# Kernel optimization log

Measured on AMD Instinct MI355X. Metric: run time of the kernel, lower is better.

## Reference

```python
import jax, jax.numpy as jnp
import numpy as np

T, B, H, OUT = 64, 4096, 256, 2
SLOPE = 25.0  # snntorch surrogate.fast_sigmoid default slope


@jax.custom_vjp
def spike(x):
    # Heaviside forward, fast-sigmoid surrogate gradient backward
    return (x > 0).astype(x.dtype)

def _spk_fwd(x):
    return (x > 0).astype(x.dtype), x

def _spk_bwd(x, g):
    return (g / (SLOPE * jnp.abs(x) + 1.0) ** 2,)

spike.defvjp(_spk_fwd, _spk_bwd)


def temporal_embedding(length):
    center = length // 2
    sigma = length / 10
    pos = np.arange(length)
    e = np.exp(-0.5 * ((pos - center) / sigma) ** 2)
    e = (e - e.min()) / (e.max() - e.min())
    return jnp.asarray(e, dtype=jnp.float32)


def setup_inputs() -> dict:
    key = jax.random.key(0)
    ks = jax.random.split(key, 16)

    def lin(k, o, i):
        bound = 1.0 / np.sqrt(i)
        kw, kb = jax.random.split(k)
        W = jax.random.uniform(kw, (o, i), minval=-bound, maxval=bound, dtype=jnp.float32)
        b = jax.random.uniform(kb, (o,), minval=-bound, maxval=bound, dtype=jnp.float32)
        return W, b

    W_in, b_in = lin(ks[0], H, 3)
    W_h, b_h = lin(ks[1], H, H)
    W_h2, b_h2 = lin(ks[2], H, H)
    W_out, b_out = lin(ks[3], OUT, H)
    W_pred, b_pred = lin(ks[4], OUT, T * 4)
    u = lambda k, n: jax.random.uniform(k, (n,), dtype=jnp.float32)
    return {
        "x": jax.random.normal(ks[5], (T, B, 3), dtype=jnp.float32),
        "W_in": W_in, "b_in": b_in,
        "beta_in": u(ks[6], H), "thr_in": u(ks[7], H),
        "W_h": W_h, "b_h": b_h,
        "beta_h": u(ks[8], H), "thr_h": u(ks[9], H),
        "W_h2": W_h2, "b_h2": b_h2,
        "beta_h2": u(ks[10], H), "thr_h2": u(ks[11], H),
        "W_out": W_out, "b_out": b_out,
        "beta_out": u(ks[12], OUT),
        "W_pred": W_pred, "b_pred": b_pred,
    }


def reference(x, W_in, b_in, beta_in, thr_in, W_h, b_h, beta_h, thr_h,
              W_h2, b_h2, beta_h2, thr_h2, W_out, b_out, beta_out,
              W_pred, b_pred):
    Tn, Bsz = x.shape[0], x.shape[1]
    emb = temporal_embedding(Tn)
    x = x * emb[:, None, None]  # per-timestep Gaussian temporal weighting

    def lif(cur, mem, beta, thr):
        # snnTorch Leaky, reset_mechanism='subtract': reset from PREVIOUS mem (detached)
        reset = jax.lax.stop_gradient((mem - thr > 0).astype(cur.dtype))
        mem = jnp.clip(beta, 0.0, 1.0) * mem + cur - reset * thr
        return spike(mem - thr), mem

    def step(carry, x_t):
        m1, m2, m4, m3 = carry
        s1, m1 = lif(x_t @ W_in.T + b_in, m1, beta_in, thr_in)
        s2, m2 = lif(s1 @ W_h.T + b_h, m2, beta_h, thr_h)
        s4, m4 = lif(s2 @ W_h2.T + b_h2, m4, beta_h2, thr_h2)
        # li_out: reset_mechanism='none', default threshold=1.0
        m3 = jnp.clip(beta_out, 0.0, 1.0) * m3 + s4 @ W_out.T + b_out
        spk_out = spike(m3 - 1.0)
        return (m1, m2, m4, m3), (spk_out, m3)

    z = lambda n: jnp.zeros((Bsz, n), x.dtype)
    init = (z(W_in.shape[0]), z(W_h.shape[0]), z(W_h2.shape[0]), z(W_out.shape[0]))
    _, (spk_rec, mem_rec) = jax.lax.scan(step, init, x)
    out = jnp.concatenate([spk_rec, mem_rec], axis=-1)  # [T, B, 2*OUT]
    # torch .view(B, T*2*OUT) on contiguous [T,B,2*OUT] == plain reshape
    out = out.reshape(Bsz, Tn * out.shape[-1])
    return out @ W_pred.T + b_pred  # [B, OUT]
```

## Files before the change

### kernel.cpp

```cpp
#include <hip/hip_runtime.h>
#include <hip/hip_bf16.h>

#define TT 64
#define BB 4096
#define HH 256
#define BMb 16
#define NBLK (BB / BMb)

typedef short bf16x8_t __attribute__((ext_vector_type(8)));
typedef float f32x4_t  __attribute__((ext_vector_type(4)));

#define WS_WA_B   0u
#define WS_EMB_B  786432u
#define WS_REC_B  1048576u

__device__ __forceinline__ float clip01f(float v) {
    return fminf(fmaxf(v, 0.0f), 1.0f);
}

__global__ __launch_bounds__(64) void setup_emb_kernel(float* __restrict__ emb) {
    int i = threadIdx.x;
    const double sigma = 64.0 / 10.0;
    const double c = 32.0;
    double d = ((double)i - c) / sigma;
    double e = exp(-0.5 * (d * d));
    double d0 = (0.0 - c) / sigma;
    double emin = exp(-0.5 * (d0 * d0));
    emb[i] = (float)((e - emin) / (1.0 - emin));
}

__global__ __launch_bounds__(256) void split_weights_kernel(
    const float* __restrict__ W_h, const float* __restrict__ W_h2,
    unsigned short* __restrict__ WA)
{
    int flat = blockIdx.x * 256 + threadIdx.x;
    int j     = flat & 7;
    int lane  = (flat >> 3) & 63;
    int ntile = (flat >> 9) & 15;
    int kt    = (flat >> 13) & 7;
    int rest  = flat >> 16;
    int part  = rest % 3;
    int layer = rest / 3;
    int k = kt * 32 + (lane >> 4) * 8 + j;
    int n = ntile * 16 + (lane & 15);
    const float* W = layer ? W_h2 : W_h;
    float w = W[n * HH + k];
    __hip_bfloat16 h = __float2bfloat16(w);
    float r1 = w - __bfloat162float(h);
    __hip_bfloat16 m = __float2bfloat16(r1);
    float r2 = r1 - __bfloat162float(m);
    __hip_bfloat16 l = __float2bfloat16(r2);
    __hip_bfloat16 v = (part == 0) ? h : ((part == 1) ? m : l);
    WA[flat] = *reinterpret_cast<unsigned short*>(&v);
}

union U16x8 { uint4 u; bf16x8_t v; };


#define AS1 __attribute__((address_space(1)))
#define AS3 __attribute__((address_space(3)))
__device__ __forceinline__ void gl16(const void* g, void* l) {
    __builtin_amdgcn_global_load_lds((AS1 const void*)g, (AS3 void*)l, 16, 0, 0);
}

#define ISSUE6(Wc, ktn, sl) do {                                               \
    const char* gb_ = (const char*)(Wc) + (ktn) * 16384;                       \
    char* lb_ = myring + (sl) * 6144;                                          \
    gl16(gb_,          lb_);                                                   \
    gl16(gb_ + 1024,   lb_ + 1024);                                            \
    gl16(gb_ + 131072, lb_ + 2048);                                            \
    gl16(gb_ + 132096, lb_ + 3072);                                            \
    gl16(gb_ + 262144, lb_ + 4096);                                            \
    gl16(gb_ + 263168, lb_ + 5120);                                            \
} while (0)

#define STEPD2(sl, Bp, ktb, Wi, kti, D0, D1) do {                              \
    asm volatile("s_waitcnt vmcnt(6)" ::: "memory");                           \
    __builtin_amdgcn_sched_barrier(0);                                         \
    U16x8 br_, a0_, a1_, a2_, b0_, b1_, b2_;                                   \
    br_.u = (Bp)[(ktb) * 64];                               \
    a0_.u = ringRd[(sl) * 384 + 0];                                            \
    b0_.u = ringRd[(sl) * 384 + 64];                                           \
    a1_.u = ringRd[(sl) * 384 + 128];                                          \
    b1_.u = ringRd[(sl) * 384 + 192];                                          \
    a2_.u = ringRd[(sl) * 384 + 256];                                          \
    b2_.u = ringRd[(sl) * 384 + 320];                                          \
    asm volatile("s_waitcnt lgkmcnt(0)" ::: "memory");                         \
    __builtin_amdgcn_sched_barrier(0);                                         \
    ISSUE6(Wi, kti, sl);                                                       \
    __builtin_amdgcn_sched_barrier(0);                                         \
    D0 = __builtin_amdgcn_mfma_f32_16x16x32_bf16(a0_.v, br_.v, D0, 0, 0, 0);   \
    D0 = __builtin_amdgcn_mfma_f32_16x16x32_bf16(a1_.v, br_.v, D0, 0, 0, 0);   \
    D0 = __builtin_amdgcn_mfma_f32_16x16x32_bf16(a2_.v, br_.v, D0, 0, 0, 0);   \
    D1 = __builtin_amdgcn_mfma_f32_16x16x32_bf16(b0_.v, br_.v, D1, 0, 0, 0);   \
    D1 = __builtin_amdgcn_mfma_f32_16x16x32_bf16(b1_.v, br_.v, D1, 0, 0, 0);   \
    D1 = __builtin_amdgcn_mfma_f32_16x16x32_bf16(b2_.v, br_.v, D1, 0, 0, 0);   \
} while (0)

#define GPHASE(Wc, Wn, Bp, D0, D1) do {                                        \
    STEPD2(0, Bp, 0, Wc, 2, D0, D1);                                           \
    STEPD2(1, Bp, 1, Wc, 3, D0, D1);                                           \
    STEPD2(0, Bp, 2, Wc, 4, D0, D1);                                           \
    STEPD2(1, Bp, 3, Wc, 5, D0, D1);                                           \
    STEPD2(0, Bp, 4, Wc, 6, D0, D1);                                           \
    STEPD2(1, Bp, 5, Wc, 7, D0, D1);                                           \
    STEPD2(0, Bp, 6, Wn, 0, D0, D1);                                           \
    STEPD2(1, Bp, 7, Wn, 1, D0, D1);                                           \
} while (0)

__device__ __forceinline__ void li_walker(
    const float* __restrict__ WoutS, const float (*__restrict__ S3F)[260],
    int wb, int ooc, float bto, float bo, float& m3s,
    float* __restrict__ rec, int t, int b0, int lane)
{
    if (lane < 32) {
        const float* wrow = WoutS + ooc * HH;
        const float* srow = S3F[wb];
        float p = 0.f;
#pragma unroll 8
        for (int k4 = 0; k4 < 64; ++k4) {
            float4 sv = *(const float4*)(srow + k4 * 4);
            float4 wv = *(const float4*)(wrow + k4 * 4);
            p = fmaf(sv.x, wv.x, p);
            p = fmaf(sv.y, wv.y, p);
            p = fmaf(sv.z, wv.z, p);
            p = fmaf(sv.w, wv.w, p);
        }
        float mm3 = fmaf(bto, m3s, p);
        mm3 = mm3 + bo;
        m3s = mm3;
        float spk = ((m3s - 1.0f) > 0.f) ? 1.f : 0.f;
        float om3 = __shfl_xor(m3s, 16, 64);
        float osp = __shfl_xor(spk, 16, 64);
        if (lane < 16) {
            *(float4*)(rec + ((size_t)t * BB + b0 + wb) * 4) =
                make_float4(spk, osp, m3s, om3);
        }
    }
}

__global__ __launch_bounds__(512) void snn_main_kernel(
    const float* __restrict__ x,
    const float* __restrict__ W_in, const float* __restrict__ b_in,
    const float* __restrict__ beta_in, const float* __restrict__ thr_in,
    const float* __restrict__ b_h, const float* __restrict__ beta_h, const float* __restrict__ thr_h,
    const float* __restrict__ b_h2, const float* __restrict__ beta_h2, const float* __restrict__ thr_h2,
    const float* __restrict__ W_out, const float* __restrict__ b_out, const float* __restrict__ beta_out,
    const unsigned short* __restrict__ WA, const float* __restrict__ emb,
    float* __restrict__ rec)
{
#pragma clang fp contract(off)
    const int tid = threadIdx.x;
    const int w = tid >> 6;
    const int lane = tid & 63;
    const int b = lane & 15;
    const int g = lane >> 4;
    const int b0 = blockIdx.x * BMb;

    __shared__ unsigned short sbuf1[8 * 64 * 8];
    __shared__ unsigned short sbuf2[8 * 64 * 8];
    __shared__ __align__(16) float S3F[16][260];
    __shared__ __align__(16) float WoutS[2 * HH];
    __shared__ float4 PL1a[HH];
    __shared__ float2 PL1b[HH];
    __shared__ float4 PL2[HH];
    __shared__ float4 PL3[HH];
    __shared__ float  xs[TT][BMb][3];
    __shared__ float  embS[TT];
    __shared__ __align__(16) char ring[8 * 2 * 6144];

    char* myring = ring + w * 12288;
    const uint4* ringRd = (const uint4*)(ring + w * 12288 + lane * 16);

    WoutS[tid] = W_out[tid];
    if (tid < HH) {
        int n = tid;
        PL1a[n] = make_float4(W_in[n * 3], W_in[n * 3 + 1], W_in[n * 3 + 2], b_in[n]);
        PL1b[n] = make_float2(clip01f(beta_in[n]), thr_in[n]);
        PL2[n]  = make_float4(b_h[n],  clip01f(beta_h[n]),  thr_h[n],  0.f);
        PL3[n]  = make_float4(b_h2[n], clip01f(beta_h2[n]), thr_h2[n], 0.f);
    }
    if (tid < TT) embS[tid] = emb[tid];
#pragma unroll
    for (int i = tid; i < TT * BMb; i += 512) {
        int ts = i >> 4, bb = i & 15;
        const float* xp = x + ((size_t)ts * BB + b0 + bb) * 3;
        xs[ts][bb][0] = xp[0];
        xs[ts][bb][1] = xp[1];
        xs[ts][bb][2] = xp[2];
    }

    const int nb0 = w * 32 + g * 4;

    float m1[2][4], m2[2][4], m4[2][4];
#pragma unroll
    for (int u = 0; u < 2; ++u)
#pragma unroll
        for (int r = 0; r < 4; ++r) { m1[u][r] = 0.f; m2[u][r] = 0.f; m4[u][r] = 0.f; }

    const int sb0 = ((w * 64 + ((g >> 1) * 16 + b)) * 8 + (g & 1) * 4);

    const int wb = lane & 15;
    const int ooc = (lane >> 4) & 1;
    float bto = clip01f(beta_out[ooc]);
    float bo = b_out[ooc];
    float m3s = 0.f;

    const uint4* W2 = (const uint4*)WA + (size_t)(2 * w) * 64 + lane;
    const uint4* W3 = W2 + 24576;
    const uint4* Bp1 = (const uint4*)sbuf1 + lane;
    const uint4* Bp2 = (const uint4*)sbuf2 + lane;

    ISSUE6(W2, 0, 0);
    ISSUE6(W2, 1, 1);

    __syncthreads();

    for (int t = 0; t < TT; ++t) {
        {
            float et = embS[t];
            float xe0 = xs[t][b][0] * et;
            float xe1 = xs[t][b][1] * et;
            float xe2 = xs[t][b][2] * et;
            unsigned sp[2][4];
#pragma unroll
            for (int u = 0; u < 2; ++u)
#pragma unroll
            for (int r = 0; r < 4; ++r) {
                int n = nb0 + u * 16 + r;
                float4 pa = PL1a[n];
                float2 pb = PL1b[n];
                float a1 = xe0 * pa.x;
                a1 = fmaf(xe1, pa.y, a1);
                a1 = fmaf(xe2, pa.z, a1);
                float cur = a1 + pa.w;
                float rf = ((m1[u][r] - pb.y) > 0.f) ? 1.f : 0.f;
                float mm = fmaf(pb.x, m1[u][r], cur);
                mm = fmaf(-rf, pb.y, mm);
                m1[u][r] = mm;
                sp[u][r] = ((mm - pb.y) > 0.f) ? 0x3F80u : 0u;
            }
            *(uint2*)(sbuf1 + sb0)       = make_uint2(sp[0][0] | (sp[0][1] << 16), sp[0][2] | (sp[0][3] << 16));
            *(uint2*)(sbuf1 + sb0 + 256) = make_uint2(sp[1][0] | (sp[1][1] << 16), sp[1][2] | (sp[1][3] << 16));
        }
        __syncthreads();

        if (w == 0 && t > 0)
            li_walker(WoutS, S3F, wb, ooc, bto, bo, m3s, rec, t - 1, b0, lane);
        {
            f32x4_t D0 = (f32x4_t){0.f, 0.f, 0.f, 0.f};
            f32x4_t D1 = (f32x4_t){0.f, 0.f, 0.f, 0.f};
            GPHASE(W2, W3, Bp1, D0, D1);
            unsigned sp[2][4];
#pragma unroll
            for (int r = 0; r < 4; ++r) {
                int n0 = nb0 + r;
                float4 p2 = PL2[n0];
                float cur = D0[r] + p2.x;
                float rf = ((m2[0][r] - p2.z) > 0.f) ? 1.f : 0.f;
                float mm = fmaf(p2.y, m2[0][r], cur);
                mm = fmaf(-rf, p2.z, mm);
                m2[0][r] = mm;
                sp[0][r] = ((mm - p2.z) > 0.f) ? 0x3F80u : 0u;
            }
#pragma unroll
            for (int r = 0; r < 4; ++r) {
                int n1 = nb0 + 16 + r;
                float4 p2 = PL2[n1];
                float cur = D1[r] + p2.x;
                float rf = ((m2[1][r] - p2.z) > 0.f) ? 1.f : 0.f;
                float mm = fmaf(p2.y, m2[1][r], cur);
                mm = fmaf(-rf, p2.z, mm);
                m2[1][r] = mm;
                sp[1][r] = ((mm - p2.z) > 0.f) ? 0x3F80u : 0u;
            }
            *(uint2*)(sbuf2 + sb0)       = make_uint2(sp[0][0] | (sp[0][1] << 16), sp[0][2] | (sp[0][3] << 16));
            *(uint2*)(sbuf2 + sb0 + 256) = make_uint2(sp[1][0] | (sp[1][1] << 16), sp[1][2] | (sp[1][3] << 16));
        }
        __syncthreads();

        {
            f32x4_t E0 = (f32x4_t){0.f, 0.f, 0.f, 0.f};
            f32x4_t E1 = (f32x4_t){0.f, 0.f, 0.f, 0.f};
            GPHASE(W3, W2, Bp2, E0, E1);
            float s3v[2][4];
#pragma unroll
            for (int r = 0; r < 4; ++r) {
                int n0 = nb0 + r;
                float4 p3 = PL3[n0];
                float cur = E0[r] + p3.x;
                float rf = ((m4[0][r] - p3.z) > 0.f) ? 1.f : 0.f;
                float mm = fmaf(p3.y, m4[0][r], cur);
                mm = fmaf(-rf, p3.z, mm);
                m4[0][r] = mm;
                s3v[0][r] = ((mm - p3.z) > 0.f) ? 1.0f : 0.0f;
            }
#pragma unroll
            for (int r = 0; r < 4; ++r) {
                int n1 = nb0 + 16 + r;
                float4 p3 = PL3[n1];
                float cur = E1[r] + p3.x;
                float rf = ((m4[1][r] - p3.z) > 0.f) ? 1.f : 0.f;
                float mm = fmaf(p3.y, m4[1][r], cur);
                mm = fmaf(-rf, p3.z, mm);
                m4[1][r] = mm;
                s3v[1][r] = ((mm - p3.z) > 0.f) ? 1.0f : 0.0f;
            }
            *(float4*)(&S3F[b][nb0])      = make_float4(s3v[0][0], s3v[0][1], s3v[0][2], s3v[0][3]);
            *(float4*)(&S3F[b][nb0 + 16]) = make_float4(s3v[1][0], s3v[1][1], s3v[1][2], s3v[1][3]);
        }
        __syncthreads();
    }

    if (w == 0)
        li_walker(WoutS, S3F, wb, ooc, bto, bo, m3s, rec, TT - 1, b0, lane);
}

__global__ __launch_bounds__(256) void pred_kernel(
    const float* __restrict__ rec, const float* __restrict__ W_pred,
    const float* __restrict__ b_pred, float* __restrict__ out)
{
#pragma clang fp contract(off)
    int r = blockIdx.x * 256 + threadIdx.x;
    const float* f = rec + (size_t)r * 256;
    float a0 = 0.f, a1 = 0.f;
#pragma unroll 4
    for (int c = 0; c < 256; ++c) {
        float v = f[c];
        a0 = fmaf(v, W_pred[c], a0);
        a1 = fmaf(v, W_pred[256 + c], a1);
    }
    out[r * 2 + 0] = a0 + b_pred[0];
    out[r * 2 + 1] = a1 + b_pred[1];
}

extern "C" void kernel_launch(void* const* d_in, const int* in_sizes, int n_in,
                              void* d_out, int out_size, void* d_ws, size_t ws_size,
                              hipStream_t stream)
{
    const float* x        = (const float*)d_in[0];
    const float* W_in     = (const float*)d_in[1];
    const float* b_in     = (const float*)d_in[2];
    const float* beta_in  = (const float*)d_in[3];
    const float* thr_in   = (const float*)d_in[4];
    const float* W_h      = (const float*)d_in[5];
    const float* b_h      = (const float*)d_in[6];
    const float* beta_h   = (const float*)d_in[7];
    const float* thr_h    = (const float*)d_in[8];
    const float* W_h2     = (const float*)d_in[9];
    const float* b_h2     = (const float*)d_in[10];
    const float* beta_h2  = (const float*)d_in[11];
    const float* thr_h2   = (const float*)d_in[12];
    const float* W_out    = (const float*)d_in[13];
    const float* b_out    = (const float*)d_in[14];
    const float* beta_out = (const float*)d_in[15];
    const float* W_pred   = (const float*)d_in[16];
    const float* b_pred   = (const float*)d_in[17];

    char* ws = (char*)d_ws;
    unsigned short* WA = (unsigned short*)(ws + WS_WA_B);
    float* emb = (float*)(ws + WS_EMB_B);
    float* rec = (float*)(ws + WS_REC_B);

    split_weights_kernel<<<1536, 256, 0, stream>>>(W_h, W_h2, WA);
    setup_emb_kernel<<<1, 64, 0, stream>>>(emb);

    snn_main_kernel<<<NBLK, 512, 0, stream>>>(
        x, W_in, b_in, beta_in, thr_in,
        b_h, beta_h, thr_h,
        b_h2, beta_h2, thr_h2,
        W_out, b_out, beta_out,
        WA, emb, rec);

    pred_kernel<<<BB / 256, 256, 0, stream>>>(rec, W_pred, b_pred, (float*)d_out);
}
```

Before: 741.9 us.

## Batch four timesteps per weight stream and pack layer-3 spikes as ballot bitmasks

Processes timesteps in chunks of four so that each weight tile streamed from global memory into the LDS ring is reused for four MFMA sets. This amortises weight traffic and cuts the number of barriers per step. Layer-3 spikes are now stored as wave ballot bitmasks rather than a float matrix, and the output LI walker decodes those bits serially, four timesteps at a time. The costs are more accumulator registers, an extra barrier per chunk, and a slower scalar bit-decoding loop in wave 0.

```diff
diff --git a/kernel.cpp b/kernel.cpp
--- a/kernel.cpp
+++ b/kernel.cpp
@@ -6,6 +6,8 @@
 #define HH 256
 #define BMb 16
 #define NBLK (BB / BMb)
+#define TC 4
+#define NCH (TT / TC)
 
 typedef short bf16x8_t __attribute__((ext_vector_type(8)));
 typedef float f32x4_t  __attribute__((ext_vector_type(4)));
@@ -74,57 +76,58 @@
     gl16(gb_ + 263168, lb_ + 5120);                                            \
 } while (0)
 
-#define STEPD2(sl, Bp, ktb, Wi, kti, D0, D1) do {                              \
+#define STEPT(sl, ktb, Wi, kti) do {                                           \
     asm volatile("s_waitcnt vmcnt(6)" ::: "memory");                           \
     __builtin_amdgcn_sched_barrier(0);                                         \
-    U16x8 br_, a0_, a1_, a2_, b0_, b1_, b2_;                                   \
-    br_.u = (Bp)[(ktb) * 64];                               \
-    a0_.u = ringRd[(sl) * 384 + 0];                                            \
-    b0_.u = ringRd[(sl) * 384 + 64];                                           \
-    a1_.u = ringRd[(sl) * 384 + 128];                                          \
-    b1_.u = ringRd[(sl) * 384 + 192];                                          \
-    a2_.u = ringRd[(sl) * 384 + 256];                                          \
-    b2_.u = ringRd[(sl) * 384 + 320];                                          \
+    U16x8 wa0_, wa1_, wa2_, wb0_, wb1_, wb2_;                                  \
+    wa0_.u = ringRd[(sl) * 384 + 0];                                           \
+    wb0_.u = ringRd[(sl) * 384 + 64];                                          \
+    wa1_.u = ringRd[(sl) * 384 + 128];                                         \
+    wb1_.u = ringRd[(sl) * 384 + 192];                                         \
+    wa2_.u = ringRd[(sl) * 384 + 256];                                         \
+    wb2_.u = ringRd[(sl) * 384 + 320];                                         \
     asm volatile("s_waitcnt lgkmcnt(0)" ::: "memory");                         \
     __builtin_amdgcn_sched_barrier(0);                                         \
     ISSUE6(Wi, kti, sl);                                                       \
     __builtin_amdgcn_sched_barrier(0);                                         \
-    D0 = __builtin_amdgcn_mfma_f32_16x16x32_bf16(a0_.v, br_.v, D0, 0, 0, 0);   \
-    D0 = __builtin_amdgcn_mfma_f32_16x16x32_bf16(a1_.v, br_.v, D0, 0, 0, 0);   \
-    D0 = __builtin_amdgcn_mfma_f32_16x16x32_bf16(a2_.v, br_.v, D0, 0, 0, 0);   \
-    D1 = __builtin_amdgcn_mfma_f32_16x16x32_bf16(b0_.v, br_.v, D1, 0, 0, 0);   \
-    D1 = __builtin_amdgcn_mfma_f32_16x16x32_bf16(b1_.v, br_.v, D1, 0, 0, 0);   \
-    D1 = __builtin_amdgcn_mfma_f32_16x16x32_bf16(b2_.v, br_.v, D1, 0, 0, 0);   \
+    _Pragma("unroll")                                                          \
+    for (int tt_ = 0; tt_ < TC; ++tt_) {                                       \
+        U16x8 br_; br_.u = BfL[tt_ * 512 + (ktb) * 64];                        \
+        D0[tt_] = __builtin_amdgcn_mfma_f32_16x16x32_bf16(wa0_.v, br_.v, D0[tt_], 0, 0, 0); \
+        D0[tt_] = __builtin_amdgcn_mfma_f32_16x16x32_bf16(wa1_.v, br_.v, D0[tt_], 0, 0, 0); \
+        D0[tt_] = __builtin_amdgcn_mfma_f32_16x16x32_bf16(wa2_.v, br_.v, D0[tt_], 0, 0, 0); \
+        D1[tt_] = __builtin_amdgcn_mfma_f32_16x16x32_bf16(wb0_.v, br_.v, D1[tt_], 0, 0, 0); \
+        D1[tt_] = __builtin_amdgcn_mfma_f32_16x16x32_bf16(wb1_.v, br_.v, D1[tt_], 0, 0, 0); \
+        D1[tt_] = __builtin_amdgcn_mfma_f32_16x16x32_bf16(wb2_.v, br_.v, D1[tt_], 0, 0, 0); \
+    }                                                                          \
 } while (0)
 
-#define GPHASE(Wc, Wn, Bp, D0, D1) do {                                        \
-    STEPD2(0, Bp, 0, Wc, 2, D0, D1);                                           \
-    STEPD2(1, Bp, 1, Wc, 3, D0, D1);                                           \
-    STEPD2(0, Bp, 2, Wc, 4, D0, D1);                                           \
-    STEPD2(1, Bp, 3, Wc, 5, D0, D1);                                           \
-    STEPD2(0, Bp, 4, Wc, 6, D0, D1);                                           \
-    STEPD2(1, Bp, 5, Wc, 7, D0, D1);                                           \
-    STEPD2(0, Bp, 6, Wn, 0, D0, D1);                                           \
-    STEPD2(1, Bp, 7, Wn, 1, D0, D1);                                           \
+#define GPHASE(Wc, Wn) do {                                                    \
+    STEPT(0, 0, Wc, 2);                                                        \
+    STEPT(1, 1, Wc, 3);                                                        \
+    STEPT(0, 2, Wc, 4);                                                        \
+    STEPT(1, 3, Wc, 5);                                                        \
+    STEPT(0, 4, Wc, 6);                                                        \
+    STEPT(1, 5, Wc, 7);                                                        \
+    STEPT(0, 6, Wn, 0);                                                        \
+    STEPT(1, 7, Wn, 1);                                                        \
 } while (0)
 
-__device__ __forceinline__ void li_walker(
-    const float* __restrict__ WoutS, const float (*__restrict__ S3F)[260],
+__device__ __forceinline__ void li_walker_bits(
+    const float* __restrict__ WoutS, const unsigned long long (*__restrict__ M3Lt)[4],
     int wb, int ooc, float bto, float bo, float& m3s,
     float* __restrict__ rec, int t, int b0, int lane)
 {
     if (lane < 32) {
-        const float* wrow = WoutS + ooc * HH;
-        const float* srow = S3F[wb];
         float p = 0.f;
-#pragma unroll 8
-        for (int k4 = 0; k4 < 64; ++k4) {
-            float4 sv = *(const float4*)(srow + k4 * 4);
-            float4 wv = *(const float4*)(wrow + k4 * 4);
-            p = fmaf(sv.x, wv.x, p);
-            p = fmaf(sv.y, wv.y, p);
-            p = fmaf(sv.z, wv.z, p);
-            p = fmaf(sv.w, wv.w, p);
+        for (int k = 0; k < HH; ++k) {
+            int ww = k >> 4, gg = (k >> 2) & 3, reg = k & 3;
+            unsigned long long word = M3Lt[ww][reg];
+            unsigned w32 = (gg < 2) ? (unsigned)word : (unsigned)(word >> 32);
+            int sh = ((gg & 1) << 4) | wb;
+            unsigned bit = (w32 >> sh) & 1u;
+            float wv = WoutS[ooc * HH + k];
+            p = p + (bit ? wv : 0.f);
         }
         float mm3 = fmaf(bto, m3s, p);
         mm3 = mm3 + bo;
@@ -157,9 +160,8 @@
     const int g = lane >> 4;
     const int b0 = blockIdx.x * BMb;
 
-    __shared__ unsigned short sbuf1[8 * 64 * 8];
-    __shared__ unsigned short sbuf2[8 * 64 * 8];
-    __shared__ __align__(16) float S3F[16][260];
+    __shared__ __align__(16) unsigned short frag[TC][8 * 64 * 8];
+    __shared__ unsigned long long M3L[TC][16][4];
     __shared__ __align__(16) float WoutS[2 * HH];
     __shared__ float4 PL1a[HH];
     __shared__ float2 PL1b[HH];
@@ -171,6 +173,7 @@
 
     char* myring = ring + w * 12288;
     const uint4* ringRd = (const uint4*)(ring + w * 12288 + lane * 16);
+    const uint4* BfL = (const uint4*)frag + lane;
 
     WoutS[tid] = W_out[tid];
     if (tid < HH) {
@@ -208,16 +211,19 @@
 
     const uint4* W2 = (const uint4*)WA + (size_t)(2 * w) * 64 + lane;
     const uint4* W3 = W2 + 24576;
-    const uint4* Bp1 = (const uint4*)sbuf1 + lane;
-    const uint4* Bp2 = (const uint4*)sbuf2 + lane;
 
     ISSUE6(W2, 0, 0);
     ISSUE6(W2, 1, 1);
 
     __syncthreads();
 
-    for (int t = 0; t < TT; ++t) {
-        {
+#pragma unroll 1
+    for (int c = 0; c < NCH; ++c) {
+        const int t0 = c * TC;
+
+#pragma unroll
+        for (int tt = 0; tt < TC; ++tt) {
+            const int t = t0 + tt;
             float et = embS[t];
             float xe0 = xs[t][b][0] * et;
             float xe1 = xs[t][b][1] * et;
@@ -240,23 +246,35 @@
                 m1[u][r] = mm;
                 sp[u][r] = ((mm - pb.y) > 0.f) ? 0x3F80u : 0u;
             }
-            *(uint2*)(sbuf1 + sb0)       = make_uint2(sp[0][0] | (sp[0][1] << 16), sp[0][2] | (sp[0][3] << 16));
-            *(uint2*)(sbuf1 + sb0 + 256) = make_uint2(sp[1][0] | (sp[1][1] << 16), sp[1][2] | (sp[1][3] << 16));
+            *(uint2*)(&frag[tt][sb0])       = make_uint2(sp[0][0] | (sp[0][1] << 16), sp[0][2] | (sp[0][3] << 16));
+            *(uint2*)(&frag[tt][sb0 + 256]) = make_uint2(sp[1][0] | (sp[1][1] << 16), sp[1][2] | (sp[1][3] << 16));
         }
         __syncthreads();
 
-        if (w == 0 && t > 0)
-            li_walker(WoutS, S3F, wb, ooc, bto, bo, m3s, rec, t - 1, b0, lane);
-        {
-            f32x4_t D0 = (f32x4_t){0.f, 0.f, 0.f, 0.f};
-            f32x4_t D1 = (f32x4_t){0.f, 0.f, 0.f, 0.f};
-            GPHASE(W2, W3, Bp1, D0, D1);
+        if (w == 0 && c > 0) {
+#pragma unroll
+            for (int tt = 0; tt < TC; ++tt)
+                li_walker_bits(WoutS, M3L[tt], wb, ooc, bto, bo, m3s,
+                               rec, t0 - TC + tt, b0, lane);
+        }
+
+        f32x4_t D0[TC], D1[TC];
+#pragma unroll
+        for (int tt = 0; tt < TC; ++tt) {
+            D0[tt] = (f32x4_t){0.f, 0.f, 0.f, 0.f};
+            D1[tt] = (f32x4_t){0.f, 0.f, 0.f, 0.f};
+        }
+        GPHASE(W2, W3);
+
+        uint2 s2w[TC][2];
+#pragma unroll
+        for (int tt = 0; tt < TC; ++tt) {
             unsigned sp[2][4];
 #pragma unroll
             for (int r = 0; r < 4; ++r) {
                 int n0 = nb0 + r;
                 float4 p2 = PL2[n0];
-                float cur = D0[r] + p2.x;
+                float cur = D0[tt][r] + p2.x;
                 float rf = ((m2[0][r] - p2.z) > 0.f) ? 1.f : 0.f;
                 float mm = fmaf(p2.y, m2[0][r], cur);
                 mm = fmaf(-rf, p2.z, mm);
@@ -267,53 +285,60 @@
             for (int r = 0; r < 4; ++r) {
                 int n1 = nb0 + 16 + r;
                 float4 p2 = PL2[n1];
-                float cur = D1[r] + p2.x;
+                float cur = D1[tt][r] + p2.x;
                 float rf = ((m2[1][r] - p2.z) > 0.f) ? 1.f : 0.f;
                 float mm = fmaf(p2.y, m2[1][r], cur);
                 mm = fmaf(-rf, p2.z, mm);
                 m2[1][r] = mm;
                 sp[1][r] = ((mm - p2.z) > 0.f) ? 0x3F80u : 0u;
             }
-            *(uint2*)(sbuf2 + sb0)       = make_uint2(sp[0][0] | (sp[0][1] << 16), sp[0][2] | (sp[0][3] << 16));
-            *(uint2*)(sbuf2 + sb0 + 256) = make_uint2(sp[1][0] | (sp[1][1] << 16), sp[1][2] | (sp[1][3] << 16));
+            s2w[tt][0] = make_uint2(sp[0][0] | (sp[0][1] << 16), sp[0][2] | (sp[0][3] << 16));
+            s2w[tt][1] = make_uint2(sp[1][0] | (sp[1][1] << 16), sp[1][2] | (sp[1][3] << 16));
         }
         __syncthreads();
 
-        {
-            f32x4_t E0 = (f32x4_t){0.f, 0.f, 0.f, 0.f};
-            f32x4_t E1 = (f32x4_t){0.f, 0.f, 0.f, 0.f};
-            GPHASE(W3, W2, Bp2, E0, E1);
-            float s3v[2][4];
-#pragma unroll
-            for (int r = 0; r < 4; ++r) {
-                int n0 = nb0 + r;
-                float4 p3 = PL3[n0];
-                float cur = E0[r] + p3.x;
-                float rf = ((m4[0][r] - p3.z) > 0.f) ? 1.f : 0.f;
-                float mm = fmaf(p3.y, m4[0][r], cur);
-                mm = fmaf(-rf, p3.z, mm);
-                m4[0][r] = mm;
-                s3v[0][r] = ((mm - p3.z) > 0.f) ? 1.0f : 0.0f;
+#pragma unroll
+        for (int tt = 0; tt < TC; ++tt) {
+            *(uint2*)(&frag[tt][sb0])       = s2w[tt][0];
+            *(uint2*)(&frag[tt][sb0 + 256]) = s2w[tt][1];
+        }
+        __syncthreads();
+
+#pragma unroll
+        for (int tt = 0; tt < TC; ++tt) {
+            D0[tt] = (f32x4_t){0.f, 0.f, 0.f, 0.f};
+            D1[tt] = (f32x4_t){0.f, 0.f, 0.f, 0.f};
+        }
+        GPHASE(W3, W2);
+
+#pragma unroll
+        for (int tt = 0; tt < TC; ++tt) {
+#pragma unroll
+            for (int u = 0; u < 2; ++u) {
+#pragma unroll
+                for (int r = 0; r < 4; ++r) {
+                    int n = nb0 + u * 16 + r;
+                    float4 p3 = PL3[n];
+                    float cur = ((u == 0) ? D0[tt][r] : D1[tt][r]) + p3.x;
+                    float rf = ((m4[u][r] - p3.z) > 0.f) ? 1.f : 0.f;
+                    float mm = fmaf(p3.y, m4[u][r], cur);
+                    mm = fmaf(-rf, p3.z, mm);
+                    m4[u][r] = mm;
+                    bool s3 = (mm - p3.z) > 0.f;
+                    unsigned long long mk = __ballot(s3);
+                    if (lane == 0) M3L[tt][2 * w + u][r] = mk;
+                }
             }
-#pragma unroll
-            for (int r = 0; r < 4; ++r) {
-                int n1 = nb0 + 16 + r;
-                float4 p3 = PL3[n1];
-                float cur = E1[r] + p3.x;
-                float rf = ((m4[1][r] - p3.z) > 0.f) ? 1.f : 0.f;
-                float mm = fmaf(p3.y, m4[1][r], cur);
-                mm = fmaf(-rf, p3.z, mm);
-                m4[1][r] = mm;
-                s3v[1][r] = ((mm - p3.z) > 0.f) ? 1.0f : 0.0f;
-            }
-            *(float4*)(&S3F[b][nb0])      = make_float4(s3v[0][0], s3v[0][1], s3v[0][2], s3v[0][3]);
-            *(float4*)(&S3F[b][nb0 + 16]) = make_float4(s3v[1][0], s3v[1][1], s3v[1][2], s3v[1][3]);
         }
         __syncthreads();
     }
 
-    if (w == 0)
-        li_walker(WoutS, S3F, wb, ooc, bto, bo, m3s, rec, TT - 1, b0, lane);
+    if (w == 0) {
+#pragma unroll
+        for (int tt = 0; tt < TC; ++tt)
+            li_walker_bits(WoutS, M3L[tt], wb, ooc, bto, bo, m3s,
+                           rec, TT - TC + tt, b0, lane);
+    }
 }
 
 __global__ __launch_bounds__(256) void pred_kernel(
```

Measured after the change: 993.2 us. 1.34x slower.
